# Performance work log

Measured on AMD Instinct MI355X. Metric: run time of the kernel, lower is better.

## Reference

```python
import jax, jax.numpy as jnp
import numpy as np
from jax import lax

# Fixed image shape (H, W) for all images, standard detection resize
H_IMG, W_IMG = 800.0, 1333.0
SCORE_THRESH = 0.05
NMS_THRESH = 0.5
DET_PER_IMG = 100
K_PRE = 2048  # NMS candidate budget per image (after score threshold)
BBOX_XFORM_CLIP = float(np.log(1000.0 / 16.0))
WX, WY, WW, WH = 10.0, 10.0, 5.0, 5.0  # bbox_reg_weights


def setup_inputs() -> dict:
    B, P, C = 8, 2000, 81
    key = jax.random.key(0)
    k1, k2, k3, k4 = jax.random.split(key, 4)
    class_logits = 2.0 * jax.random.normal(k1, (B * P, C), jnp.float32)
    box_regression = 0.5 * jax.random.normal(k2, (B * P, C * 4), jnp.float32)
    # valid proposal boxes inside the image: (x1,y1) + (w,h)
    xy = jax.random.uniform(k3, (B, P, 2), jnp.float32) * jnp.array([W_IMG - 128.0, H_IMG - 128.0], jnp.float32)
    wh = 1.0 + 127.0 * jax.random.uniform(k4, (B, P, 2), jnp.float32)
    proposals = jnp.concatenate([xy, xy + wh], axis=-1)
    return {"class_logits": class_logits, "box_regression": box_regression, "proposals": proposals}


def _decode(rel, boxes):
    # BoxCoder.decode: rel [N, C, 4], boxes [N, 4] -> [N, C, 4]
    w = boxes[:, 2] - boxes[:, 0]
    h = boxes[:, 3] - boxes[:, 1]
    cx = boxes[:, 0] + 0.5 * w
    cy = boxes[:, 1] + 0.5 * h
    dx = rel[..., 0] / WX
    dy = rel[..., 1] / WY
    dw = jnp.minimum(rel[..., 2] / WW, BBOX_XFORM_CLIP)
    dh = jnp.minimum(rel[..., 3] / WH, BBOX_XFORM_CLIP)
    pcx = dx * w[:, None] + cx[:, None]
    pcy = dy * h[:, None] + cy[:, None]
    pw = jnp.exp(dw) * w[:, None]
    ph = jnp.exp(dh) * h[:, None]
    return jnp.stack([pcx - 0.5 * pw, pcy - 0.5 * ph, pcx + 0.5 * pw, pcy + 0.5 * ph], axis=-1)


def _pairwise_iou(b):
    # b: [K, 4] -> [K, K]
    area = jnp.maximum(b[:, 2] - b[:, 0], 0.0) * jnp.maximum(b[:, 3] - b[:, 1], 0.0)
    lt = jnp.maximum(b[:, None, :2], b[None, :, :2])
    rb = jnp.minimum(b[:, None, 2:], b[None, :, 2:])
    wh = jnp.maximum(rb - lt, 0.0)
    inter = wh[..., 0] * wh[..., 1]
    union = area[:, None] + area[None, :] - inter
    return inter / jnp.maximum(union, 1e-9)


def _greedy_nms(boxes, valid):
    # boxes: [K, 4] sorted by score desc; valid: [K] bool. Exact greedy NMS.
    K = boxes.shape[0]
    iou = _pairwise_iou(boxes)
    idx = jnp.arange(K)

    def body(i, keep):
        sup = keep[i] & (iou[i] > NMS_THRESH) & (idx > i)
        return keep & ~sup

    return lax.fori_loop(0, K, body, valid)


def reference(class_logits, box_regression, proposals):
    B, P, _ = proposals.shape
    C = class_logits.shape[-1]
    # decode all class-specific boxes, softmax scores
    rel = box_regression.reshape(-1, C, 4)
    pred = _decode(rel, proposals.reshape(-1, 4)).reshape(B, P, C, 4)
    scores = jax.nn.softmax(class_logits, axis=-1).reshape(B, P, C)
    # drop background class 0
    M = P * (C - 1)
    boxes = pred[:, :, 1:, :].reshape(B, M, 4)
    scores = scores[:, :, 1:].reshape(B, M)
    labels = jnp.broadcast_to(jnp.arange(1, C)[None, None, :], (B, P, C - 1)).reshape(B, M)
    # clip to image
    x1 = jnp.clip(boxes[..., 0], 0.0, W_IMG)
    y1 = jnp.clip(boxes[..., 1], 0.0, H_IMG)
    x2 = jnp.clip(boxes[..., 2], 0.0, W_IMG)
    y2 = jnp.clip(boxes[..., 3], 0.0, H_IMG)
    boxes = jnp.stack([x1, y1, x2, y2], axis=-1)
    # score threshold + remove_small_boxes(min_size=0.01), as a validity mask
    valid = (scores > SCORE_THRESH) & ((x2 - x1) >= 0.01) & ((y2 - y1) >= 0.01)
    masked = jnp.where(valid, scores, -1.0)
    # top-K candidates per image (sorted desc -> NMS visiting order)
    top_s, top_i = lax.top_k(masked, K_PRE)
    top_b = jnp.take_along_axis(boxes, top_i[..., None], axis=1)
    top_l = jnp.take_along_axis(labels, top_i, axis=1)
    top_v = top_s > 0.0
    # batched_nms: per-class coordinate offsets so classes never overlap
    off = top_l.astype(jnp.float32) * (jnp.maximum(W_IMG, H_IMG) + 1.0)
    keep = jax.vmap(_greedy_nms)(top_b + off[..., None], top_v)
    final = jnp.where(keep, top_s, -1.0)
    det_s, det_i = lax.top_k(final, DET_PER_IMG)
    det_b = jnp.take_along_axis(top_b, det_i[..., None], axis=1)
    det_l = jnp.take_along_axis(top_l, det_i, axis=1)
    det_valid = det_s > 0.0  # padding slots have score -1
    return det_b, det_s, det_l, det_valid
```

## Files before the change

kernel.cpp:

```cpp
#include <hip/hip_runtime.h>
#include <cstdint>
#include <cstddef>

typedef unsigned long long u64;

constexpr int Bn   = 8;
constexpr int Pn   = 2000;
constexpr int Cn   = 81;
constexpr int CM1  = 80;
constexpr int Mn   = Pn * CM1;
constexpr int KPRE = 2048;
constexpr int NDET = 100;
constexpr int CAP  = 4096;
constexpr int NBINS = 5632;
constexpr int BINOFF = (122 << 10);
constexpr int NCH  = 64;
constexpr int CHEL = Mn / NCH;
constexpr int WCOLS = 256;
constexpr float W_IMG = 1333.0f;
constexpr float H_IMG = 800.0f;
constexpr float XFORM_CLIP = 4.135166556742356f;
constexpr float NMS_OFF = 1334.0f;

constexpr size_t OFF_HIST  = 0;
constexpr size_t ZERO_BYTES = (size_t)Bn * NBINS * 4;
constexpr size_t OFF_CNT   = ZERO_BYTES;
constexpr size_t OFF_T     = OFF_CNT + Bn * 4;
constexpr size_t OFF_BC    = OFF_T + Bn * 4;
constexpr size_t OFF_SCORE = OFF_BC + (size_t)Bn * NCH * 4;
constexpr size_t OFF_CANDA = OFF_SCORE + (size_t)Bn * Mn * 4;
constexpr size_t OFF_CANDB = OFF_CANDA + (size_t)Bn * CAP * 8;
constexpr size_t OFF_FINAL = OFF_CANDB + (size_t)Bn * CAP * 8;

__device__ __forceinline__ void decode_clip(const float4 rv, float w, float h,
                                            float cx, float cy, float out[4]) {
  float dx = rv.x / 10.0f;
  float dy = rv.y / 10.0f;
  float dw = fminf(rv.z / 5.0f, XFORM_CLIP);
  float dh = fminf(rv.w / 5.0f, XFORM_CLIP);
  float pcx = dx * w + cx;
  float pcy = dy * h + cy;
  float pw = expf(dw) * w;
  float ph = expf(dh) * h;
  out[0] = fminf(fmaxf(pcx - 0.5f * pw, 0.0f), W_IMG);
  out[1] = fminf(fmaxf(pcy - 0.5f * ph, 0.0f), H_IMG);
  out[2] = fminf(fmaxf(pcx + 0.5f * pw, 0.0f), W_IMG);
  out[3] = fminf(fmaxf(pcy + 0.5f * ph, 0.0f), H_IMG);
}

__device__ __forceinline__ int score_bin(unsigned bits) {
  int bin = (int)(bits >> 13) - BINOFF;
  return min(max(bin, 0), NBINS - 1);
}

__global__ __launch_bounds__(256) void
k1_score(const float* __restrict__ logits, const float* __restrict__ reg,
         const float* __restrict__ props, float* __restrict__ scores,
         int* __restrict__ hist) {
  int wid = blockIdx.x * 4 + (threadIdx.x >> 6);
  int lane = threadIdx.x & 63;
  if (wid >= Bn * Pn) return;
  int b = wid / Pn, p = wid % Pn;

  const float* lg = logits + (size_t)wid * Cn;
  float x0 = lg[lane];
  float x1 = (lane < Cn - 64) ? lg[64 + lane] : -3.4e38f;
  float mx = fmaxf(x0, x1);
  for (int m = 32; m; m >>= 1) mx = fmaxf(mx, __shfl_xor(mx, m, 64));
  float e0 = expf(x0 - mx);
  float e1 = (lane < Cn - 64) ? expf(x1 - mx) : 0.0f;
  float ssum = e0 + e1;
  for (int m = 32; m; m >>= 1) ssum += __shfl_xor(ssum, m, 64);

  const float4 pb = *reinterpret_cast<const float4*>(props + (size_t)wid * 4);
  float w = pb.z - pb.x, h = pb.w - pb.y;
  float cx = pb.x + 0.5f * w, cy = pb.y + 0.5f * h;

  const float* rrow = reg + (size_t)wid * (Cn * 4);
  float* srow = scores + (size_t)b * Mn + (size_t)p * CM1;
  int* hrow = hist + (size_t)b * NBINS;

  #pragma unroll
  for (int slot = 0; slot < 2; slot++) {
    int c = lane + slot * 64;
    float e = slot ? e1 : e0;
    if (c < 1 || c >= Cn) continue;
    float sc = e / ssum;
    float4 rv = *reinterpret_cast<const float4*>(rrow + c * 4);
    float bx[4];
    decode_clip(rv, w, h, cx, cy, bx);
    bool valid = (sc > 0.05f) && (bx[2] - bx[0] >= 0.01f) && (bx[3] - bx[1] >= 0.01f);
    srow[c - 1] = valid ? sc : -1.0f;
    if (valid) atomicAdd(&hrow[score_bin(__float_as_uint(sc))], 1);
  }
}

__global__ __launch_bounds__(256) void
k2_thresh(const int* __restrict__ hist, int* __restrict__ T) {
  int b = blockIdx.x, t = threadIdx.x;
  __shared__ int partial[256];
  __shared__ int sufAfter[256];
  __shared__ int tmax;
  const int CH = NBINS / 256;
  const int* hrow = hist + (size_t)b * NBINS;
  int lo = t * CH, hi = lo + CH;
  int s = 0;
  for (int i = lo; i < hi; i++) s += hrow[i];
  partial[t] = s;
  if (t == 0) tmax = 0;
  __syncthreads();
  if (t == 0) {
    int acc = 0;
    for (int q = 255; q >= 0; q--) { sufAfter[q] = acc; acc += partial[q]; }
  }
  __syncthreads();
  int cum = sufAfter[t];
  int cand = -1;
  for (int i = hi - 1; i >= lo; i--) {
    cum += hrow[i];
    if (cum >= KPRE) { cand = i; break; }
  }
  if (cand >= 0) atomicMax(&tmax, cand);
  __syncthreads();
  if (t == 0) T[b] = tmax;
}

__global__ __launch_bounds__(256) void
k3a_count(const float* __restrict__ scores, const int* __restrict__ T,
          int* __restrict__ bcount) {
  int blk = blockIdx.x, t = threadIdx.x, lane = t & 63, w = t >> 6;
  int b = blk / NCH, c = blk % NCH;
  int Tb = T[b];
  int cntl = 0;
  #pragma unroll
  for (int it = 0; it < 10; it++) {
    int il = it * 256 + t;
    if (il < CHEL) {
      float sc = scores[(size_t)b * Mn + c * CHEL + il];
      if (sc > 0.0f && score_bin(__float_as_uint(sc)) >= Tb) cntl++;
    }
  }
  for (int s = 32; s; s >>= 1) cntl += __shfl_xor(cntl, s, 64);
  __shared__ int wsum[4];
  if (lane == 0) wsum[w] = cntl;
  __syncthreads();
  if (t == 0) bcount[blk] = wsum[0] + wsum[1] + wsum[2] + wsum[3];
}

__global__ __launch_bounds__(256) void
k3c_scatter(const float* __restrict__ scores, const int* __restrict__ T,
            const int* __restrict__ bcount, int* __restrict__ cnt,
            u64* __restrict__ candA) {
  int blk = blockIdx.x, t = threadIdx.x, lane = t & 63, w = t >> 6;
  int b = blk / NCH, c = blk % NCH;
  __shared__ int sbase;
  __shared__ int wc[4];
  if (t < 64) {
    int v = bcount[b * NCH + t];
    int incl = v;
    for (int s = 1; s < 64; s <<= 1) {
      int y = __shfl_up(incl, s, 64);
      if (t >= s) incl += y;
    }
    int excl = incl - v;
    int basec = __shfl(excl, c, 64);
    int total = __shfl(incl, 63, 64);
    if (t == 0) {
      sbase = basec;
      if (c == NCH - 1) cnt[b] = total;
    }
  }
  __syncthreads();
  int base = sbase;
  int Tb = T[b];
  for (int it = 0; it < 10; it++) {
    int il = it * 256 + t;
    int m = c * CHEL + il;
    bool pass = false;
    unsigned bits = 0;
    if (il < CHEL) {
      float sc = scores[(size_t)b * Mn + m];
      bits = __float_as_uint(sc);
      pass = (sc > 0.0f) && (score_bin(bits) >= Tb);
    }
    u64 bal = __ballot(pass);
    if (lane == 0) wc[w] = __popcll(bal);
    __syncthreads();
    int off = base;
    for (int q = 0; q < w; q++) off += wc[q];
    int tot = wc[0] + wc[1] + wc[2] + wc[3];
    int rank = __popcll(bal & ((1ull << lane) - 1ull));
    int pos = off + rank;
    if (pass && pos < CAP)
      candA[(size_t)b * CAP + pos] =
          ((u64)bits << 32) | (unsigned)(0xFFFFFFFFu - (unsigned)m);
    base += tot;
    __syncthreads();
  }
}

__global__ __launch_bounds__(256) void
k4a_chunk(u64* __restrict__ candA, const int* __restrict__ cnt) {
  __shared__ u64 sk[512];
  int blk = blockIdx.x, t = threadIdx.x;
  int b = blk >> 3, ch = blk & 7;
  int n = min(cnt[b], CAP);
  int base = ch * 512;
  #pragma unroll
  for (int i = t; i < 512; i += 256) {
    int g = base + i;
    sk[i] = (g < n) ? candA[(size_t)b * CAP + g] : 0ull;
  }
  __syncthreads();
  for (int k = 2; k <= 512; k <<= 1) {
    for (int j = k >> 1; j > 0; j >>= 1) {
      #pragma unroll
      for (int i = t; i < 512; i += 256) {
        int ixj = i ^ j;
        if (ixj > i) {
          u64 a = sk[i], c2 = sk[ixj];
          bool dir = ((i & k) == 0);
          if ((a < c2) == dir) { sk[i] = c2; sk[ixj] = a; }
        }
      }
      __syncthreads();
    }
  }
  #pragma unroll
  for (int i = t; i < 512; i += 256)
    candA[(size_t)b * CAP + base + i] = sk[i];
}

__global__ __launch_bounds__(256) void
k4b_merge(const u64* __restrict__ in, u64* __restrict__ out, int LA, int LOUT,
          int mPerImg, int inImgStride, int outImgStride) {
  extern __shared__ u64 sm[];
  int blk = blockIdx.x, t = threadIdx.x;
  int b = blk / mPerImg, m = blk % mPerImg;
  const u64* A = in + (size_t)b * inImgStride + (size_t)m * 2 * LA;
  u64* O = out + (size_t)b * outImgStride + (size_t)m * LOUT;
  int LB = LA, LT = 2 * LA;
  for (int i = t; i < LT; i += 256) sm[i] = A[i];
  __syncthreads();
  const u64* sA = sm;
  const u64* sB = sm + LA;
  int CH = LOUT / 256;
  int d = t * CH;
  int lo = max(0, d - LB), hi = min(d, LA);
  while (lo < hi) {
    int mid = (lo + hi) >> 1;
    if (sA[mid] >= sB[d - 1 - mid]) lo = mid + 1; else hi = mid;
  }
  int i = lo, j = d - lo;
  for (int e = 0; e < CH; e++) {
    u64 v;
    if (j >= LB || (i < LA && sA[i] >= sB[j])) v = sA[i++];
    else v = sB[j++];
    O[d + e] = v;
  }
}

__device__ __forceinline__ void key_decode(u64 key, int b,
                                           const float* __restrict__ reg,
                                           const float* __restrict__ props,
                                           float bx[4], int& label, float& sc) {
  sc = __uint_as_float((unsigned)(key >> 32));
  bx[0] = bx[1] = bx[2] = bx[3] = 0.0f;
  label = 0;
  if (key != 0ull) {
    int m = (int)(0xFFFFFFFFu - (unsigned)key);
    int p = m / CM1;
    int c = m - p * CM1 + 1;
    int nidx = b * Pn + p;
    const float4 pb = *reinterpret_cast<const float4*>(props + (size_t)nidx * 4);
    float w = pb.z - pb.x, h = pb.w - pb.y;
    float cx = pb.x + 0.5f * w, cy = pb.y + 0.5f * h;
    float4 rv = *reinterpret_cast<const float4*>(reg + (size_t)nidx * (Cn * 4) + c * 4);
    decode_clip(rv, w, h, cx, cy, bx);
    label = c;
  }
}

__global__ __launch_bounds__(1024) void
k5_nms(const u64* __restrict__ fin,
       const float* __restrict__ reg, const float* __restrict__ props,
       float* __restrict__ out) {
  int b = blockIdx.x, t = threadIdx.x, lane = t & 63, w = t >> 6;
  __shared__ float4 obox[KPRE];
  __shared__ float  sar[KPRE];
  __shared__ u64 mask[WCOLS][4];
  __shared__ u64 keepw[KPRE / 64];
  __shared__ int acc[NDET];
  __shared__ int kcnt_sh;

  #pragma unroll
  for (int s = 0; s < 2; s++) {
    int j = t + s * 1024;
    u64 key = fin[(size_t)b * KPRE + j];
    float bx[4]; int label; float sc;
    key_decode(key, b, reg, props, bx, label, sc);
    float off = (float)label * NMS_OFF;
    float4 ob = {bx[0] + off, bx[1] + off, bx[2] + off, bx[3] + off};
    obox[j] = ob;
    sar[j] = fmaxf(bx[2] - bx[0], 0.0f) * fmaxf(bx[3] - bx[1], 0.0f);
    u64 bal = __ballot(key != 0ull);
    if (lane == 0) keepw[s * 16 + w] = bal;
  }
  __syncthreads();

  int kcount = 0;
  for (int w0 = 0; w0 < KPRE && kcount < NDET; w0 += WCOLS) {
    if (w0 > 0 && kcount > 0) {
      if (t < WCOLS) {
        int j = w0 + t;
        u64 kwv = keepw[j >> 6];
        bool alive = (kwv >> (j & 63)) & 1ull;
        if (alive) {
          float4 jb = obox[j];
          float jar = sar[j];
          for (int a = 0; a < kcount; a++) {
            int ii = acc[a];
            float4 ab = obox[ii];
            float ix1 = fmaxf(ab.x, jb.x), iy1 = fmaxf(ab.y, jb.y);
            float ix2 = fminf(ab.z, jb.z), iy2 = fminf(ab.w, jb.w);
            float iw = fmaxf(ix2 - ix1, 0.0f), ih = fmaxf(iy2 - iy1, 0.0f);
            float inter = iw * ih;
            if (inter > 0.0f) {
              float iou = inter / fmaxf(sar[ii] + jar - inter, 1e-9f);
              if (iou > 0.5f) { alive = false; break; }
            }
          }
        }
        u64 bal = __ballot(alive);
        if (lane == 0) keepw[(w0 >> 6) + (t >> 6)] = bal;
      }
      __syncthreads();
    }
    {
      int r = t >> 2, wd = t & 3;
      int rg = w0 + r;
      float4 rb = obox[rg];
      float rar = sar[rg];
      u64 m = 0;
      int cbase = w0 + wd * 64;
      for (int jj = 0; jj < 64; jj++) {
        int cg = cbase + jj;
        float4 cb = obox[cg];
        float ix1 = fmaxf(rb.x, cb.x), iy1 = fmaxf(rb.y, cb.y);
        float ix2 = fminf(rb.z, cb.z), iy2 = fminf(rb.w, cb.w);
        float iw = fmaxf(ix2 - ix1, 0.0f), ih = fmaxf(iy2 - iy1, 0.0f);
        float inter = iw * ih;
        if (inter > 0.0f && cg > rg) {
          float iou = inter / fmaxf(rar + sar[cg] - inter, 1e-9f);
          if (iou > 0.5f) m |= (1ull << jj);
        }
      }
      mask[r][wd] = m;
    }
    __syncthreads();
    if (w == 0) {
      u64 kw0 = keepw[(w0 >> 6) + 0];
      u64 kw1 = keepw[(w0 >> 6) + 1];
      u64 kw2 = keepw[(w0 >> 6) + 2];
      u64 kw3 = keepw[(w0 >> 6) + 3];
      int kc = kcount;
      #pragma unroll
      for (int wq = 0; wq < 4; wq++) {
        u64 cw = (wq == 0) ? kw0 : (wq == 1) ? kw1 : (wq == 2) ? kw2 : kw3;
        if (cw == 0ull) continue;
        for (int rb0 = 0; rb0 < 64 && kc < NDET; rb0 += 4) {
          u64 gbits = (cw >> rb0) & 0xFull;
          int r = wq * 64 + rb0;
          u64 rm0a = mask[r][0],   rm0b = mask[r][1],   rm0c = mask[r][2],   rm0d = mask[r][3];
          u64 rm1a = mask[r+1][0], rm1b = mask[r+1][1], rm1c = mask[r+1][2], rm1d = mask[r+1][3];
          u64 rm2a = mask[r+2][0], rm2b = mask[r+2][1], rm2c = mask[r+2][2], rm2d = mask[r+2][3];
          u64 rm3a = mask[r+3][0], rm3b = mask[r+3][1], rm3c = mask[r+3][2], rm3d = mask[r+3][3];
          if (gbits == 0ull) continue;
          #pragma unroll
          for (int d = 0; d < 4; d++) {
            u64 cwq = (wq == 0) ? kw0 : (wq == 1) ? kw1 : (wq == 2) ? kw2 : kw3;
            if ((cwq >> (rb0 + d)) & 1ull) {
              if (lane == 0) acc[kc] = w0 + r + d;
              kc++;
              if (kc >= NDET) break;
              u64 ma = (d == 0) ? rm0a : (d == 1) ? rm1a : (d == 2) ? rm2a : rm3a;
              u64 mb = (d == 0) ? rm0b : (d == 1) ? rm1b : (d == 2) ? rm2b : rm3b;
              u64 mc = (d == 0) ? rm0c : (d == 1) ? rm1c : (d == 2) ? rm2c : rm3c;
              u64 md = (d == 0) ? rm0d : (d == 1) ? rm1d : (d == 2) ? rm2d : rm3d;
              kw0 &= ~ma; kw1 &= ~mb; kw2 &= ~mc; kw3 &= ~md;
            }
          }
          cw = (wq == 0) ? kw0 : (wq == 1) ? kw1 : (wq == 2) ? kw2 : kw3;
        }
      }
      if (lane == 0) {
        keepw[(w0 >> 6) + 0] = kw0;
        keepw[(w0 >> 6) + 1] = kw1;
        keepw[(w0 >> 6) + 2] = kw2;
        keepw[(w0 >> 6) + 3] = kw3;
        kcnt_sh = kc;
      }
    }
    __syncthreads();
    kcount = kcnt_sh;
  }

  if (t == 0 && kcount < NDET) {
    int run = kcount;
    for (int wq = 0; wq < KPRE / 64 && run < NDET; wq++) {
      u64 nk = ~keepw[wq];
      while (nk && run < NDET) {
        int bit2 = __ffsll((long long)nk) - 1;
        nk &= nk - 1;
        acc[run++] = wq * 64 + bit2;
      }
    }
  }
  __syncthreads();

  if (t < NDET) {
    int k = acc[t];
    bool kept = t < kcount;
    u64 key = fin[(size_t)b * KPRE + k];
    float bx[4]; int label; float sc;
    key_decode(key, b, reg, props, bx, label, sc);
    int oi = b * NDET + t;
    out[(size_t)oi * 4 + 0] = bx[0];
    out[(size_t)oi * 4 + 1] = bx[1];
    out[(size_t)oi * 4 + 2] = bx[2];
    out[(size_t)oi * 4 + 3] = bx[3];
    out[Bn * NDET * 4 + oi] = kept ? sc : -1.0f;
    out[Bn * NDET * 5 + oi] = (float)label;
    out[Bn * NDET * 6 + oi] = kept ? 1.0f : 0.0f;
  }
}

extern "C" void kernel_launch(void* const* d_in, const int* in_sizes, int n_in,
                              void* d_out, int out_size, void* d_ws, size_t ws_size,
                              hipStream_t stream) {
  const float* logits = (const float*)d_in[0];
  const float* reg    = (const float*)d_in[1];
  const float* props  = (const float*)d_in[2];
  float* out = (float*)d_out;
  char* ws = (char*)d_ws;

  int*   hist   = (int*)(ws + OFF_HIST);
  int*   cnt    = (int*)(ws + OFF_CNT);
  int*   T      = (int*)(ws + OFF_T);
  int*   bcount = (int*)(ws + OFF_BC);
  float* scores = (float*)(ws + OFF_SCORE);
  u64*   candA  = (u64*)(ws + OFF_CANDA);
  u64*   candB  = (u64*)(ws + OFF_CANDB);
  u64*   fin    = (u64*)(ws + OFF_FINAL);

  hipMemsetAsync(ws + OFF_HIST, 0, ZERO_BYTES, stream);
  k1_score<<<(Bn * Pn) / 4, 256, 0, stream>>>(logits, reg, props, scores, hist);
  k2_thresh<<<Bn, 256, 0, stream>>>(hist, T);
  k3a_count<<<Bn * NCH, 256, 0, stream>>>(scores, T, bcount);
  k3c_scatter<<<Bn * NCH, 256, 0, stream>>>(scores, T, bcount, cnt, candA);
  k4a_chunk<<<Bn * 8, 256, 0, stream>>>(candA, cnt);
  k4b_merge<<<Bn * 4, 256, 1024 * 8, stream>>>(candA, candB, 512, 1024, 4, CAP, CAP);
  k4b_merge<<<Bn * 2, 256, 2048 * 8, stream>>>(candB, candA, 1024, 2048, 2, CAP, CAP);
  k4b_merge<<<Bn * 1, 256, 4096 * 8, stream>>>(candA, fin, 2048, 2048, 1, CAP, KPRE);
  k5_nms<<<Bn, 1024, 0, stream>>>(fin, reg, props, out);
}
```

Baseline: 153.0 us.

## Replace histogram top-K selection with per-section sorts merged inside NMS

The scoring kernel now writes packed score/index keys, with zero marking an invalid entry, instead of scores plus a global histogram. A new kernel compacts and bitonic-sorts each of 16 proposal sections per image in shared memory and keeps the top 2048. The NMS kernel first merges the 16 sorted lists sequentially in LDS, then runs NMS with 256 threads instead of 1024. This drops the memset, the histogram atomics, the threshold, count and scatter passes and the multi-kernel merge chain, going from many launches to three. The cost is a serial 15-step merge on only 8 blocks, less NMS parallelism, 8-byte key traffic, and no bounds check on the 4096-entry section buffer.

```diff
diff --git a/kernel.cpp b/kernel.cpp
--- a/kernel.cpp
+++ b/kernel.cpp
@@ -11,26 +11,18 @@
 constexpr int Mn   = Pn * CM1;
 constexpr int KPRE = 2048;
 constexpr int NDET = 100;
-constexpr int CAP  = 4096;
-constexpr int NBINS = 5632;
-constexpr int BINOFF = (122 << 10);
-constexpr int NCH  = 64;
-constexpr int CHEL = Mn / NCH;
-constexpr int WCOLS = 256;
+constexpr int NSEC = 16;
+constexpr int SPROP = Pn / NSEC;
+constexpr int SECEL = SPROP * CM1;
+constexpr int CBUF = 4096;
 constexpr float W_IMG = 1333.0f;
 constexpr float H_IMG = 800.0f;
 constexpr float XFORM_CLIP = 4.135166556742356f;
 constexpr float NMS_OFF = 1334.0f;
 
-constexpr size_t OFF_HIST  = 0;
-constexpr size_t ZERO_BYTES = (size_t)Bn * NBINS * 4;
-constexpr size_t OFF_CNT   = ZERO_BYTES;
-constexpr size_t OFF_T     = OFF_CNT + Bn * 4;
-constexpr size_t OFF_BC    = OFF_T + Bn * 4;
-constexpr size_t OFF_SCORE = OFF_BC + (size_t)Bn * NCH * 4;
-constexpr size_t OFF_CANDA = OFF_SCORE + (size_t)Bn * Mn * 4;
-constexpr size_t OFF_CANDB = OFF_CANDA + (size_t)Bn * CAP * 8;
-constexpr size_t OFF_FINAL = OFF_CANDB + (size_t)Bn * CAP * 8;
+constexpr size_t OFF_KEYS  = 0;
+constexpr size_t OFF_SLIST = OFF_KEYS + (size_t)Bn * Mn * 8;
+constexpr size_t OFF_SCNT  = OFF_SLIST + (size_t)Bn * NSEC * KPRE * 8;
 
 __device__ __forceinline__ void decode_clip(const float4 rv, float w, float h,
                                             float cx, float cy, float out[4]) {
@@ -48,18 +40,11 @@
   out[3] = fminf(fmaxf(pcy + 0.5f * ph, 0.0f), H_IMG);
 }
 
-__device__ __forceinline__ int score_bin(unsigned bits) {
-  int bin = (int)(bits >> 13) - BINOFF;
-  return min(max(bin, 0), NBINS - 1);
-}
-
 __global__ __launch_bounds__(256) void
 k1_score(const float* __restrict__ logits, const float* __restrict__ reg,
-         const float* __restrict__ props, float* __restrict__ scores,
-         int* __restrict__ hist) {
+         const float* __restrict__ props, u64* __restrict__ keys) {
   int wid = blockIdx.x * 4 + (threadIdx.x >> 6);
   int lane = threadIdx.x & 63;
-  if (wid >= Bn * Pn) return;
   int b = wid / Pn, p = wid % Pn;
 
   const float* lg = logits + (size_t)wid * Cn;
@@ -77,8 +62,7 @@
   float cx = pb.x + 0.5f * w, cy = pb.y + 0.5f * h;
 
   const float* rrow = reg + (size_t)wid * (Cn * 4);
-  float* srow = scores + (size_t)b * Mn + (size_t)p * CM1;
-  int* hrow = hist + (size_t)b * NBINS;
+  u64* krow = keys + (size_t)b * Mn + (size_t)p * CM1;
 
   #pragma unroll
   for (int slot = 0; slot < 2; slot++) {
@@ -90,174 +74,73 @@
     float bx[4];
     decode_clip(rv, w, h, cx, cy, bx);
     bool valid = (sc > 0.05f) && (bx[2] - bx[0] >= 0.01f) && (bx[3] - bx[1] >= 0.01f);
-    srow[c - 1] = valid ? sc : -1.0f;
-    if (valid) atomicAdd(&hrow[score_bin(__float_as_uint(sc))], 1);
+    unsigned m = (unsigned)(p * CM1 + (c - 1));
+    u64 key = valid ? (((u64)__float_as_uint(sc) << 32) | (0xFFFFFFFFu - m)) : 0ull;
+    krow[c - 1] = key;
   }
 }
 
 __global__ __launch_bounds__(256) void
-k2_thresh(const int* __restrict__ hist, int* __restrict__ T) {
-  int b = blockIdx.x, t = threadIdx.x;
-  __shared__ int partial[256];
-  __shared__ int sufAfter[256];
-  __shared__ int tmax;
-  const int CH = NBINS / 256;
-  const int* hrow = hist + (size_t)b * NBINS;
-  int lo = t * CH, hi = lo + CH;
-  int s = 0;
-  for (int i = lo; i < hi; i++) s += hrow[i];
-  partial[t] = s;
-  if (t == 0) tmax = 0;
-  __syncthreads();
-  if (t == 0) {
-    int acc = 0;
-    for (int q = 255; q >= 0; q--) { sufAfter[q] = acc; acc += partial[q]; }
-  }
-  __syncthreads();
-  int cum = sufAfter[t];
-  int cand = -1;
-  for (int i = hi - 1; i >= lo; i--) {
-    cum += hrow[i];
-    if (cum >= KPRE) { cand = i; break; }
-  }
-  if (cand >= 0) atomicMax(&tmax, cand);
-  __syncthreads();
-  if (t == 0) T[b] = tmax;
-}
-
-__global__ __launch_bounds__(256) void
-k3a_count(const float* __restrict__ scores, const int* __restrict__ T,
-          int* __restrict__ bcount) {
+k2_section(const u64* __restrict__ keys, u64* __restrict__ slist,
+           int* __restrict__ scnt) {
   int blk = blockIdx.x, t = threadIdx.x, lane = t & 63, w = t >> 6;
-  int b = blk / NCH, c = blk % NCH;
-  int Tb = T[b];
-  int cntl = 0;
-  #pragma unroll
+  int b = blk >> 4, s = blk & 15;
+  __shared__ u64 cbuf[CBUF];
+  __shared__ int wc[4];
+  const u64* kb = keys + (size_t)b * Mn + (size_t)s * SECEL;
+
+  int base = 0;
   for (int it = 0; it < 10; it++) {
-    int il = it * 256 + t;
-    if (il < CHEL) {
-      float sc = scores[(size_t)b * Mn + c * CHEL + il];
-      if (sc > 0.0f && score_bin(__float_as_uint(sc)) >= Tb) cntl++;
-    }
-  }
-  for (int s = 32; s; s >>= 1) cntl += __shfl_xor(cntl, s, 64);
-  __shared__ int wsum[4];
-  if (lane == 0) wsum[w] = cntl;
-  __syncthreads();
-  if (t == 0) bcount[blk] = wsum[0] + wsum[1] + wsum[2] + wsum[3];
-}
-
-__global__ __launch_bounds__(256) void
-k3c_scatter(const float* __restrict__ scores, const int* __restrict__ T,
-            const int* __restrict__ bcount, int* __restrict__ cnt,
-            u64* __restrict__ candA) {
-  int blk = blockIdx.x, t = threadIdx.x, lane = t & 63, w = t >> 6;
-  int b = blk / NCH, c = blk % NCH;
-  __shared__ int sbase;
-  __shared__ int wc[4];
-  if (t < 64) {
-    int v = bcount[b * NCH + t];
-    int incl = v;
-    for (int s = 1; s < 64; s <<= 1) {
-      int y = __shfl_up(incl, s, 64);
-      if (t >= s) incl += y;
-    }
-    int excl = incl - v;
-    int basec = __shfl(excl, c, 64);
-    int total = __shfl(incl, 63, 64);
-    if (t == 0) {
-      sbase = basec;
-      if (c == NCH - 1) cnt[b] = total;
-    }
-  }
-  __syncthreads();
-  int base = sbase;
-  int Tb = T[b];
-  for (int it = 0; it < 10; it++) {
-    int il = it * 256 + t;
-    int m = c * CHEL + il;
-    bool pass = false;
-    unsigned bits = 0;
-    if (il < CHEL) {
-      float sc = scores[(size_t)b * Mn + m];
-      bits = __float_as_uint(sc);
-      pass = (sc > 0.0f) && (score_bin(bits) >= Tb);
-    }
-    u64 bal = __ballot(pass);
-    if (lane == 0) wc[w] = __popcll(bal);
-    __syncthreads();
-    int off = base;
-    for (int q = 0; q < w; q++) off += wc[q];
+    int i0 = it * 1024 + t * 4;
+    u64 k0 = 0, k1 = 0, k2 = 0, k3 = 0;
+    if (i0 + 3 < SECEL) {
+      k0 = kb[i0]; k1 = kb[i0 + 1]; k2 = kb[i0 + 2]; k3 = kb[i0 + 3];
+    } else {
+      if (i0     < SECEL) k0 = kb[i0];
+      if (i0 + 1 < SECEL) k1 = kb[i0 + 1];
+      if (i0 + 2 < SECEL) k2 = kb[i0 + 2];
+      if (i0 + 3 < SECEL) k3 = kb[i0 + 3];
+    }
+    int myc = (k0 != 0) + (k1 != 0) + (k2 != 0) + (k3 != 0);
+    int incl = myc;
+    for (int sh = 1; sh < 64; sh <<= 1) {
+      int y = __shfl_up(incl, sh, 64);
+      if (lane >= sh) incl += y;
+    }
+    if (lane == 63) wc[w] = incl;
+    __syncthreads();
+    int pos = base + (incl - myc);
+    for (int q = 0; q < w; q++) pos += wc[q];
     int tot = wc[0] + wc[1] + wc[2] + wc[3];
-    int rank = __popcll(bal & ((1ull << lane) - 1ull));
-    int pos = off + rank;
-    if (pass && pos < CAP)
-      candA[(size_t)b * CAP + pos] =
-          ((u64)bits << 32) | (unsigned)(0xFFFFFFFFu - (unsigned)m);
+    if (k0) cbuf[pos++] = k0;
+    if (k1) cbuf[pos++] = k1;
+    if (k2) cbuf[pos++] = k2;
+    if (k3) cbuf[pos++] = k3;
     base += tot;
     __syncthreads();
   }
-}
-
-__global__ __launch_bounds__(256) void
-k4a_chunk(u64* __restrict__ candA, const int* __restrict__ cnt) {
-  __shared__ u64 sk[512];
-  int blk = blockIdx.x, t = threadIdx.x;
-  int b = blk >> 3, ch = blk & 7;
-  int n = min(cnt[b], CAP);
-  int base = ch * 512;
-  #pragma unroll
-  for (int i = t; i < 512; i += 256) {
-    int g = base + i;
-    sk[i] = (g < n) ? candA[(size_t)b * CAP + g] : 0ull;
-  }
-  __syncthreads();
-  for (int k = 2; k <= 512; k <<= 1) {
+  int n = base;
+  int npow = 2;
+  while (npow < n) npow <<= 1;
+  for (int i = n + t; i < npow; i += 256) cbuf[i] = 0ull;
+  __syncthreads();
+  for (int k = 2; k <= npow; k <<= 1) {
     for (int j = k >> 1; j > 0; j >>= 1) {
-      #pragma unroll
-      for (int i = t; i < 512; i += 256) {
+      for (int i = t; i < npow; i += 256) {
         int ixj = i ^ j;
         if (ixj > i) {
-          u64 a = sk[i], c2 = sk[ixj];
+          u64 a = cbuf[i], c2 = cbuf[ixj];
           bool dir = ((i & k) == 0);
-          if ((a < c2) == dir) { sk[i] = c2; sk[ixj] = a; }
+          if ((a < c2) == dir) { cbuf[i] = c2; cbuf[ixj] = a; }
         }
       }
       __syncthreads();
     }
   }
-  #pragma unroll
-  for (int i = t; i < 512; i += 256)
-    candA[(size_t)b * CAP + base + i] = sk[i];
-}
-
-__global__ __launch_bounds__(256) void
-k4b_merge(const u64* __restrict__ in, u64* __restrict__ out, int LA, int LOUT,
-          int mPerImg, int inImgStride, int outImgStride) {
-  extern __shared__ u64 sm[];
-  int blk = blockIdx.x, t = threadIdx.x;
-  int b = blk / mPerImg, m = blk % mPerImg;
-  const u64* A = in + (size_t)b * inImgStride + (size_t)m * 2 * LA;
-  u64* O = out + (size_t)b * outImgStride + (size_t)m * LOUT;
-  int LB = LA, LT = 2 * LA;
-  for (int i = t; i < LT; i += 256) sm[i] = A[i];
-  __syncthreads();
-  const u64* sA = sm;
-  const u64* sB = sm + LA;
-  int CH = LOUT / 256;
-  int d = t * CH;
-  int lo = max(0, d - LB), hi = min(d, LA);
-  while (lo < hi) {
-    int mid = (lo + hi) >> 1;
-    if (sA[mid] >= sB[d - 1 - mid]) lo = mid + 1; else hi = mid;
-  }
-  int i = lo, j = d - lo;
-  for (int e = 0; e < CH; e++) {
-    u64 v;
-    if (j >= LB || (i < LA && sA[i] >= sB[j])) v = sA[i++];
-    else v = sB[j++];
-    O[d + e] = v;
-  }
+  int outn = min(n, KPRE);
+  u64* dst = slist + (size_t)blk * KPRE;
+  for (int i = t; i < outn; i += 256) dst[i] = cbuf[i];
+  if (t == 0) scnt[blk] = outn;
 }
 
 __device__ __forceinline__ void key_decode(u64 key, int b,
@@ -281,81 +164,122 @@
   }
 }
 
-__global__ __launch_bounds__(1024) void
-k5_nms(const u64* __restrict__ fin,
-       const float* __restrict__ reg, const float* __restrict__ props,
-       float* __restrict__ out) {
+__global__ __launch_bounds__(256) void
+k3_merge_nms(const u64* __restrict__ slist, const int* __restrict__ scnt,
+             const float* __restrict__ reg, const float* __restrict__ props,
+             float* __restrict__ out) {
   int b = blockIdx.x, t = threadIdx.x, lane = t & 63, w = t >> 6;
-  __shared__ float4 obox[KPRE];
-  __shared__ float  sar[KPRE];
-  __shared__ u64 mask[WCOLS][4];
+  __shared__ u64 accK[KPRE];
+  __shared__ __align__(16) char smemraw[32768];
+  __shared__ u64 maskb[256][4];
   __shared__ u64 keepw[KPRE / 64];
   __shared__ int acc[NDET];
   __shared__ int kcnt_sh;
+  u64* L = (u64*)smemraw;
+  float4* obox = (float4*)smemraw;
+
+  int alen = scnt[b * NSEC];
+  {
+    const u64* S0 = slist + (size_t)(b * NSEC) * KPRE;
+    for (int i = t; i < KPRE; i += 256) accK[i] = (i < alen) ? S0[i] : 0ull;
+  }
+  __syncthreads();
+  for (int s2 = 1; s2 < NSEC; s2++) {
+    int nB = scnt[b * NSEC + s2];
+    const u64* B = slist + (size_t)(b * NSEC + s2) * KPRE;
+    for (int i = t; i < nB; i += 256) L[i] = B[i];
+    __syncthreads();
+    int outLen = min(KPRE, alen + nB);
+    int d = t * 8;
+    u64 rg[8];
+    int cnt = 0;
+    if (d < outLen) {
+      int lo = max(0, d - nB), hi = min(d, alen);
+      while (lo < hi) {
+        int mid = (lo + hi) >> 1;
+        if (accK[mid] >= L[d - 1 - mid]) lo = mid + 1; else hi = mid;
+      }
+      int i = lo, j = d - lo;
+      for (int e = 0; e < 8 && d + e < outLen; e++) {
+        u64 v;
+        if (j >= nB || (i < alen && accK[i] >= L[j])) v = accK[i++];
+        else v = L[j++];
+        rg[cnt++] = v;
+      }
+    }
+    __syncthreads();
+    for (int e = 0; e < cnt; e++) accK[d + e] = rg[e];
+    alen = outLen;
+    __syncthreads();
+  }
+  for (int i = alen + t; i < KPRE; i += 256) accK[i] = 0ull;
+  __syncthreads();
 
   #pragma unroll
-  for (int s = 0; s < 2; s++) {
-    int j = t + s * 1024;
-    u64 key = fin[(size_t)b * KPRE + j];
+  for (int s = 0; s < 8; s++) {
+    int j = t + s * 256;
+    u64 key = accK[j];
     float bx[4]; int label; float sc;
     key_decode(key, b, reg, props, bx, label, sc);
     float off = (float)label * NMS_OFF;
-    float4 ob = {bx[0] + off, bx[1] + off, bx[2] + off, bx[3] + off};
-    obox[j] = ob;
-    sar[j] = fmaxf(bx[2] - bx[0], 0.0f) * fmaxf(bx[3] - bx[1], 0.0f);
+    obox[j] = make_float4(bx[0] + off, bx[1] + off, bx[2] + off, bx[3] + off);
     u64 bal = __ballot(key != 0ull);
-    if (lane == 0) keepw[s * 16 + w] = bal;
+    if (lane == 0) keepw[s * 4 + w] = bal;
   }
   __syncthreads();
 
   int kcount = 0;
-  for (int w0 = 0; w0 < KPRE && kcount < NDET; w0 += WCOLS) {
+  for (int w0 = 0; w0 < KPRE && kcount < NDET; w0 += 256) {
     if (w0 > 0 && kcount > 0) {
-      if (t < WCOLS) {
-        int j = w0 + t;
-        u64 kwv = keepw[j >> 6];
-        bool alive = (kwv >> (j & 63)) & 1ull;
-        if (alive) {
-          float4 jb = obox[j];
-          float jar = sar[j];
-          for (int a = 0; a < kcount; a++) {
-            int ii = acc[a];
-            float4 ab = obox[ii];
-            float ix1 = fmaxf(ab.x, jb.x), iy1 = fmaxf(ab.y, jb.y);
-            float ix2 = fminf(ab.z, jb.z), iy2 = fminf(ab.w, jb.w);
+      int j = w0 + t;
+      u64 kwv = keepw[j >> 6];
+      bool alive = (kwv >> (j & 63)) & 1ull;
+      if (alive) {
+        float4 jb = obox[j];
+        float jar = fmaxf(jb.z - jb.x, 0.0f) * fmaxf(jb.w - jb.y, 0.0f);
+        for (int a = 0; a < kcount; a++) {
+          float4 ab = obox[acc[a]];
+          float ix1 = fmaxf(ab.x, jb.x), iy1 = fmaxf(ab.y, jb.y);
+          float ix2 = fminf(ab.z, jb.z), iy2 = fminf(ab.w, jb.w);
+          float iw = fmaxf(ix2 - ix1, 0.0f), ih = fmaxf(iy2 - iy1, 0.0f);
+          float inter = iw * ih;
+          if (inter > 0.0f) {
+            float aar = fmaxf(ab.z - ab.x, 0.0f) * fmaxf(ab.w - ab.y, 0.0f);
+            float iou = inter / fmaxf(aar + jar - inter, 1e-9f);
+            if (iou > 0.5f) { alive = false; break; }
+          }
+        }
+      }
+      u64 bal = __ballot(alive);
+      if (lane == 0) keepw[(w0 >> 6) + w] = bal;
+      __syncthreads();
+    }
+    {
+      int rgp = w0 + t;
+      bool ralive = (keepw[rgp >> 6] >> (rgp & 63)) & 1ull;
+      float4 rb = obox[rgp];
+      float rar = fmaxf(rb.z - rb.x, 0.0f) * fmaxf(rb.w - rb.y, 0.0f);
+      #pragma unroll
+      for (int wd = 0; wd < 4; wd++) {
+        u64 m = 0;
+        if (ralive) {
+          int cb0 = w0 + wd * 64;
+          for (int jj = 0; jj < 64; jj++) {
+            int cg = cb0 + jj;
+            float4 cb = obox[cg];
+            float ix1 = fmaxf(rb.x, cb.x), iy1 = fmaxf(rb.y, cb.y);
+            float ix2 = fminf(rb.z, cb.z), iy2 = fminf(rb.w, cb.w);
             float iw = fmaxf(ix2 - ix1, 0.0f), ih = fmaxf(iy2 - iy1, 0.0f);
             float inter = iw * ih;
-            if (inter > 0.0f) {
-              float iou = inter / fmaxf(sar[ii] + jar - inter, 1e-9f);
-              if (iou > 0.5f) { alive = false; break; }
+            if (inter > 0.0f && cg > rgp) {
+              float car = fmaxf(cb.z - cb.x, 0.0f) * fmaxf(cb.w - cb.y, 0.0f);
+              float iou = inter / fmaxf(rar + car - inter, 1e-9f);
+              if (iou > 0.5f) m |= (1ull << jj);
             }
           }
         }
-        u64 bal = __ballot(alive);
-        if (lane == 0) keepw[(w0 >> 6) + (t >> 6)] = bal;
-      }
-      __syncthreads();
-    }
-    {
-      int r = t >> 2, wd = t & 3;
-      int rg = w0 + r;
-      float4 rb = obox[rg];
-      float rar = sar[rg];
-      u64 m = 0;
-      int cbase = w0 + wd * 64;
-      for (int jj = 0; jj < 64; jj++) {
-        int cg = cbase + jj;
-        float4 cb = obox[cg];
-        float ix1 = fmaxf(rb.x, cb.x), iy1 = fmaxf(rb.y, cb.y);
-        float ix2 = fminf(rb.z, cb.z), iy2 = fminf(rb.w, cb.w);
-        float iw = fmaxf(ix2 - ix1, 0.0f), ih = fmaxf(iy2 - iy1, 0.0f);
-        float inter = iw * ih;
-        if (inter > 0.0f && cg > rg) {
-          float iou = inter / fmaxf(rar + sar[cg] - inter, 1e-9f);
-          if (iou > 0.5f) m |= (1ull << jj);
-        }
-      }
-      mask[r][wd] = m;
+        maskb[t][wd] = m;
+      }
     }
     __syncthreads();
     if (w == 0) {
@@ -371,10 +295,10 @@
         for (int rb0 = 0; rb0 < 64 && kc < NDET; rb0 += 4) {
           u64 gbits = (cw >> rb0) & 0xFull;
           int r = wq * 64 + rb0;
-          u64 rm0a = mask[r][0],   rm0b = mask[r][1],   rm0c = mask[r][2],   rm0d = mask[r][3];
-          u64 rm1a = mask[r+1][0], rm1b = mask[r+1][1], rm1c = mask[r+1][2], rm1d = mask[r+1][3];
-          u64 rm2a = mask[r+2][0], rm2b = mask[r+2][1], rm2c = mask[r+2][2], rm2d = mask[r+2][3];
-          u64 rm3a = mask[r+3][0], rm3b = mask[r+3][1], rm3c = mask[r+3][2], rm3d = mask[r+3][3];
+          u64 rm0a = maskb[r][0],   rm0b = maskb[r][1],   rm0c = maskb[r][2],   rm0d = maskb[r][3];
+          u64 rm1a = maskb[r+1][0], rm1b = maskb[r+1][1], rm1c = maskb[r+1][2], rm1d = maskb[r+1][3];
+          u64 rm2a = maskb[r+2][0], rm2b = maskb[r+2][1], rm2c = maskb[r+2][2], rm2d = maskb[r+2][3];
+          u64 rm3a = maskb[r+3][0], rm3b = maskb[r+3][1], rm3c = maskb[r+3][2], rm3d = maskb[r+3][3];
           if (gbits == 0ull) continue;
           #pragma unroll
           for (int d = 0; d < 4; d++) {
@@ -421,7 +345,7 @@
   if (t < NDET) {
     int k = acc[t];
     bool kept = t < kcount;
-    u64 key = fin[(size_t)b * KPRE + k];
+    u64 key = accK[k];
     float bx[4]; int label; float sc;
     key_decode(key, b, reg, props, bx, label, sc);
     int oi = b * NDET + t;
@@ -444,23 +368,11 @@
   float* out = (float*)d_out;
   char* ws = (char*)d_ws;
 
-  int*   hist   = (int*)(ws + OFF_HIST);
-  int*   cnt    = (int*)(ws + OFF_CNT);
-  int*   T      = (int*)(ws + OFF_T);
-  int*   bcount = (int*)(ws + OFF_BC);
-  float* scores = (float*)(ws + OFF_SCORE);
-  u64*   candA  = (u64*)(ws + OFF_CANDA);
-  u64*   candB  = (u64*)(ws + OFF_CANDB);
-  u64*   fin    = (u64*)(ws + OFF_FINAL);
-
-  hipMemsetAsync(ws + OFF_HIST, 0, ZERO_BYTES, stream);
-  k1_score<<<(Bn * Pn) / 4, 256, 0, stream>>>(logits, reg, props, scores, hist);
-  k2_thresh<<<Bn, 256, 0, stream>>>(hist, T);
-  k3a_count<<<Bn * NCH, 256, 0, stream>>>(scores, T, bcount);
-  k3c_scatter<<<Bn * NCH, 256, 0, stream>>>(scores, T, bcount, cnt, candA);
-  k4a_chunk<<<Bn * 8, 256, 0, stream>>>(candA, cnt);
-  k4b_merge<<<Bn * 4, 256, 1024 * 8, stream>>>(candA, candB, 512, 1024, 4, CAP, CAP);
-  k4b_merge<<<Bn * 2, 256, 2048 * 8, stream>>>(candB, candA, 1024, 2048, 2, CAP, CAP);
-  k4b_merge<<<Bn * 1, 256, 4096 * 8, stream>>>(candA, fin, 2048, 2048, 1, CAP, KPRE);
-  k5_nms<<<Bn, 1024, 0, stream>>>(fin, reg, props, out);
-}
+  u64* keys  = (u64*)(ws + OFF_KEYS);
+  u64* slist = (u64*)(ws + OFF_SLIST);
+  int* scnt  = (int*)(ws + OFF_SCNT);
+
+  k1_score<<<(Bn * Pn) / 4, 256, 0, stream>>>(logits, reg, props, keys);
+  k2_section<<<Bn * NSEC, 256, 0, stream>>>(keys, slist, scnt);
+  k3_merge_nms<<<Bn, 256, 0, stream>>>(slist, scnt, reg, props, out);
+}
```

After: 213.7 us. 39.7% more time.
